# Kernel optimization log

Measured on AMD Instinct MI355X. Metric: run time of the kernel, lower is better.

Reference implementation:

```python
import jax, jax.numpy as jnp
import numpy as np

B, C, H, W, K = 8, 768, 64, 64, 256
EPS = 1e-12  # torch F.normalize eps


def setup_inputs() -> dict:
    key = jax.random.key(0)
    k1, k2 = jax.random.split(key)
    return {
        "x": jax.random.normal(k1, (B, C, H, W), dtype=jnp.float32),
        "centroids": jax.random.normal(k2, (B, C, K), dtype=jnp.float32),
        "sim_alpha": jnp.ones((1,), dtype=jnp.float32),
        "sim_beta": jnp.zeros((1,), dtype=jnp.float32),
    }


def reference(x, centroids, sim_alpha, sim_beta):
    b, c, h, w = x.shape
    n = h * w
    x_r = x.reshape(b, c, n)               # (B,C,N)
    xt = jnp.swapaxes(x_r, 1, 2)           # (B,N,C) tokens
    ct = jnp.swapaxes(centroids, 1, 2)     # (B,K,C) centroids
    # cosine similarity (F.normalize uses max(norm, eps))
    xn = xt / jnp.maximum(jnp.linalg.norm(xt, axis=-1, keepdims=True), EPS)
    cn = ct / jnp.maximum(jnp.linalg.norm(ct, axis=-1, keepdims=True), EPS)
    cos = jnp.einsum('bkc,bnc->bkn', cn, xn)                  # (B,K,N)
    sim = jax.nn.sigmoid(sim_beta + sim_alpha * cos)          # (B,K,N)
    # hard assignment mask: each token kept only for its argmax centroid
    max_idx = jnp.argmax(sim, axis=1)                         # (B,N)
    mask = jnp.swapaxes(jax.nn.one_hot(max_idx, sim.shape[1], dtype=sim.dtype), 1, 2)  # (B,K,N)
    sim_masked = sim * mask                                   # (B,K,N)
    # aggregation: sum over tokens weighted by masked similarity
    agg = jnp.einsum('bkn,bnc->bkc', sim_masked, xt)          # (B,K,C)
    counts = jnp.sum(mask, axis=-1, keepdims=True)            # (B,K,1)
    hyperedges = (agg + ct) / (counts + 1.0)                  # (B,K,C)
    return hyperedges, sim_masked
```

## Files before the change

### kernel.cpp

```cpp
#include <hip/hip_runtime.h>
#include <cmath>

#define Bdim 8
#define Cdim 768
#define Kdim 256
#define Ndim 4096
#define NT 64
#define KC2 32
#define NCH (Cdim / KC2)

typedef __bf16 bf16x8 __attribute__((ext_vector_type(8)));
typedef short  s16x8  __attribute__((ext_vector_type(8)));
typedef float  f32x4  __attribute__((ext_vector_type(4)));
union U8 { s16x8 s; bf16x8 b; };

typedef __attribute__((address_space(1))) const unsigned int g_u32;
typedef __attribute__((address_space(3))) unsigned int l_u32;
__device__ __forceinline__ void gload16(const void* g, void* l) {
    __builtin_amdgcn_global_load_lds((g_u32*)g, (l_u32*)l, 16, 0, 0);
}

__device__ __forceinline__ unsigned short bf16_rne(float f) {
    unsigned u = __float_as_uint(f);
    unsigned r = u + 0x7FFFu + ((u >> 16) & 1u);
    return (unsigned short)(r >> 16);
}
__device__ __forceinline__ float bf2f(unsigned short h) {
    return __uint_as_float((unsigned)h << 16);
}

__device__ __forceinline__ void split3(float v, short& h, short& m, short& l) {
    unsigned u = __float_as_uint(v);
    unsigned th = u + 0x7FFFu + ((u >> 16) & 1u);
    h = (short)(th >> 16);
    float r1 = v - __uint_as_float(th & 0xFFFF0000u);
    unsigned u1 = __float_as_uint(r1);
    unsigned tm = u1 + 0x7FFFu + ((u1 >> 16) & 1u);
    m = (short)(tm >> 16);
    float r2 = r1 - __uint_as_float(tm & 0xFFFF0000u);
    unsigned u2 = __float_as_uint(r2);
    unsigned tl = u2 + 0x7FFFu + ((u2 >> 16) & 1u);
    l = (short)(tl >> 16);
}

__global__ __launch_bounds__(256) void prep_kernel(
    const float* __restrict__ cents, float* __restrict__ invc, int* __restrict__ cnt)
{
    __shared__ float red[4][Kdim];
    const int tid = threadIdx.x;
    const int b = blockIdx.x;
    const float* cb = cents + (size_t)b * Cdim * Kdim;
    const int q = tid & 63, g = tid >> 6;
    float4 ss = make_float4(0.f, 0.f, 0.f, 0.f);
    for (int r = g; r < Cdim; r += 4) {
        float4 v = *(const float4*)(cb + (size_t)r * Kdim + q * 4);
        ss.x = fmaf(v.x, v.x, ss.x); ss.y = fmaf(v.y, v.y, ss.y);
        ss.z = fmaf(v.z, v.z, ss.z); ss.w = fmaf(v.w, v.w, ss.w);
    }
    *(float4*)&red[g][q * 4] = ss;
    __syncthreads();
    float s = red[0][tid] + red[1][tid] + red[2][tid] + red[3][tid];
    invc[b * Kdim + tid] = 1.f / fmaxf(sqrtf(s), 1e-12f);
    cnt[b * Kdim + tid] = 0;
}

__global__ __launch_bounds__(256) void cvt_kernel(
    const float* __restrict__ cents, short* __restrict__ centH,
    short* __restrict__ centM, short* __restrict__ centL)
{
    const int k = threadIdx.x;
    const int bc = blockIdx.x;
    const float* src = cents + ((size_t)(bc / 96) * Cdim + (size_t)(bc % 96) * 8) * Kdim + k;
    s16x8 H, M, L;
    #pragma unroll
    for (int e = 0; e < 8; ++e) {
        short h, m, l;
        split3(src[(size_t)e * Kdim], h, m, l);
        H[e] = h; M[e] = m; L[e] = l;
    }
    ((s16x8*)centH)[(size_t)bc * 256 + k] = H;
    ((s16x8*)centM)[(size_t)bc * 256 + k] = M;
    ((s16x8*)centL)[(size_t)bc * 256 + k] = L;
}

__global__ __launch_bounds__(256) void cvt2_kernel(
    const float* __restrict__ cents, short* __restrict__ centH,
    short* __restrict__ centM, short* __restrict__ centL,
    float* __restrict__ csq)
{
    const int k = threadIdx.x;
    const int bc = blockIdx.x;
    const float* src = cents + ((size_t)(bc / 96) * Cdim + (size_t)(bc % 96) * 8) * Kdim + k;
    s16x8 H, M, L;
    float sq = 0.f;
    #pragma unroll
    for (int e = 0; e < 8; ++e) {
        float v = src[(size_t)e * Kdim];
        sq = fmaf(v, v, sq);
        short h, m, l;
        split3(v, h, m, l);
        H[e] = h; M[e] = m; L[e] = l;
    }
    ((s16x8*)centH)[(size_t)bc * 256 + k] = H;
    ((s16x8*)centM)[(size_t)bc * 256 + k] = M;
    ((s16x8*)centL)[(size_t)bc * 256 + k] = L;
    csq[(size_t)bc * 256 + k] = sq;
}

__global__ __launch_bounds__(256) void nrm_reduce_kernel(
    const float* __restrict__ csq, float* __restrict__ invc, int* __restrict__ cnt)
{
    const int k = threadIdx.x;
    const int b = blockIdx.x;
    const float* p = csq + (size_t)b * 96 * 256 + k;
    float s0 = 0.f, s1 = 0.f, s2 = 0.f, s3 = 0.f;
    #pragma unroll
    for (int j = 0; j < 96; j += 4) {
        s0 += p[(j + 0) * 256];
        s1 += p[(j + 1) * 256];
        s2 += p[(j + 2) * 256];
        s3 += p[(j + 3) * 256];
    }
    float s = ((s0 + s1) + (s2 + s3));
    invc[b * Kdim + k] = 1.f / fmaxf(sqrtf(s), 1e-12f);
    cnt[b * Kdim + k] = 0;
}

__global__ __launch_bounds__(256) void xpose3_kernel(
    const float* __restrict__ x,
    unsigned short* __restrict__ xH, unsigned short* __restrict__ xM,
    unsigned short* __restrict__ xL, float* __restrict__ xn2p)
{
    __shared__ float tile[64][68];
    __shared__ float psum[4][64];
    const int tid = threadIdx.x;
    const int bid = blockIdx.x;
    const int b  = bid / (12 * 64);
    const int r  = bid % (12 * 64);
    const int ct = r / 64, nt = r % 64;
    const float* src = x + ((size_t)b * Cdim + ct * 64) * Ndim + nt * 64;
    #pragma unroll
    for (int it = 0; it < 4; ++it) {
        int idx = tid + it * 256;
        int c = idx >> 4, n4 = idx & 15;
        *(float4*)&tile[c][n4 * 4] = *(const float4*)&src[(size_t)c * Ndim + n4 * 4];
    }
    __syncthreads();

    {
        const int grp = tid >> 6, tn = tid & 63;
        float s = 0.f;
        #pragma unroll
        for (int cc = 0; cc < 16; ++cc) {
            float v = tile[grp * 16 + cc][tn];
            s = fmaf(v, v, s);
        }
        psum[grp][tn] = s;
    }
    __syncthreads();
    if (tid < 64)
        xn2p[((size_t)(b * 12 + ct)) * Ndim + nt * 64 + tid] =
            psum[0][tid] + psum[1][tid] + psum[2][tid] + psum[3][tid];

    #pragma unroll
    for (int it = 0; it < 8; ++it) {
        int idx = tid + it * 256;
        int n = idx >> 5, cp = idx & 31;
        short h0, m0, l0, h1, m1, l1;
        split3(tile[cp * 2][n],     h0, m0, l0);
        split3(tile[cp * 2 + 1][n], h1, m1, l1);
        size_t o = ((size_t)(b * Ndim + nt * 64 + n)) * Cdim + ct * 64 + cp * 2;
        *(unsigned*)&xH[o] = (unsigned)(unsigned short)h0 | ((unsigned)(unsigned short)h1 << 16);
        *(unsigned*)&xM[o] = (unsigned)(unsigned short)m0 | ((unsigned)(unsigned short)m1 << 16);
        *(unsigned*)&xL[o] = (unsigned)(unsigned short)l0 | ((unsigned)(unsigned short)l1 << 16);
    }
}

__global__ __launch_bounds__(256) void xpose_kernel(
    const float* __restrict__ x, unsigned short* __restrict__ xTh)
{
    __shared__ float tile[64][68];
    const int tid = threadIdx.x;
    const int bid = blockIdx.x;
    const int b  = bid / (12 * 64);
    const int r  = bid % (12 * 64);
    const int ct = r / 64, nt = r % 64;
    const float* src = x + ((size_t)b * Cdim + ct * 64) * Ndim + nt * 64;
    #pragma unroll
    for (int it = 0; it < 4; ++it) {
        int idx = tid + it * 256;
        int c = idx >> 4, n4 = idx & 15;
        *(float4*)&tile[c][n4 * 4] = *(const float4*)&src[(size_t)c * Ndim + n4 * 4];
    }
    __syncthreads();
    #pragma unroll
    for (int it = 0; it < 8; ++it) {
        int idx = tid + it * 256;
        int n = idx >> 5, cp = idx & 31;
        unsigned pk = (unsigned)bf16_rne(tile[cp * 2][n])
                    | ((unsigned)bf16_rne(tile[cp * 2 + 1][n]) << 16);
        *(unsigned*)&xTh[((size_t)(b * Ndim + nt * 64 + n)) * Cdim + ct * 64 + cp * 2] = pk;
    }
}

__global__ __launch_bounds__(256) void scan_kernel(
    const int* __restrict__ cnt, const int* __restrict__ kArr,
    int* __restrict__ bucketOff, int* __restrict__ toks)
{
    __shared__ int cS[256];
    __shared__ int offS[256];
    __shared__ int cur[256];
    const int tid = threadIdx.x;
    const int b = blockIdx.x;
    cS[tid] = cnt[b * 256 + tid];
    __syncthreads();
    if (tid == 0) {
        int a = 0;
        for (int k = 0; k < 256; ++k) { offS[k] = a; a += cS[k]; }
    }
    __syncthreads();
    bucketOff[b * 256 + tid] = offS[tid];
    cur[tid] = offS[tid];
    __syncthreads();
    for (int i = tid; i < Ndim; i += 256) {
        int k = kArr[b * Ndim + i];
        int pos = atomicAdd(&cur[k], 1);
        toks[b * Ndim + pos] = i;
    }
}

__global__ __launch_bounds__(192) void aggB_kernel(
    const unsigned short* __restrict__ xTh,
    const float* __restrict__ cents,
    const float* __restrict__ wArr,
    const int* __restrict__ toks,
    const int* __restrict__ bucketOff,
    const int* __restrict__ cnt,
    float* __restrict__ hyp)
{
    const int tid = threadIdx.x;
    const int b  = blockIdx.x >> 7;
    const int kg = blockIdx.x & 127;
    const int t4 = tid * 4;
    #pragma unroll
    for (int j = 0; j < 2; ++j) {
        const int k = kg * 2 + j;
        const int off = bucketOff[b * 256 + k];
        const int num = cnt[b * 256 + k];
        const int base = b * Ndim + off;
        float a0 = 0.f, a1 = 0.f, a2 = 0.f, a3 = 0.f;
        int i = 0;
        for (; i + 4 <= num; i += 4) {
            int na = toks[base + i],     nb = toks[base + i + 1];
            int nc = toks[base + i + 2], nd = toks[base + i + 3];
            float wa = wArr[b * Ndim + na], wb = wArr[b * Ndim + nb];
            float wc = wArr[b * Ndim + nc], wd = wArr[b * Ndim + nd];
            ushort4 ha = *(const ushort4*)&xTh[((size_t)(b * Ndim + na)) * Cdim + t4];
            ushort4 hb = *(const ushort4*)&xTh[((size_t)(b * Ndim + nb)) * Cdim + t4];
            ushort4 hc = *(const ushort4*)&xTh[((size_t)(b * Ndim + nc)) * Cdim + t4];
            ushort4 hd = *(const ushort4*)&xTh[((size_t)(b * Ndim + nd)) * Cdim + t4];
            a0 += wa * bf2f(ha.x) + wb * bf2f(hb.x) + wc * bf2f(hc.x) + wd * bf2f(hd.x);
            a1 += wa * bf2f(ha.y) + wb * bf2f(hb.y) + wc * bf2f(hc.y) + wd * bf2f(hd.y);
            a2 += wa * bf2f(ha.z) + wb * bf2f(hb.z) + wc * bf2f(hc.z) + wd * bf2f(hd.z);
            a3 += wa * bf2f(ha.w) + wb * bf2f(hb.w) + wc * bf2f(hc.w) + wd * bf2f(hd.w);
        }
        for (; i < num; ++i) {
            int n = toks[base + i];
            float w = wArr[b * Ndim + n];
            ushort4 h = *(const ushort4*)&xTh[((size_t)(b * Ndim + n)) * Cdim + t4];
            a0 += w * bf2f(h.x); a1 += w * bf2f(h.y);
            a2 += w * bf2f(h.z); a3 += w * bf2f(h.w);
        }
        float d = (float)(num + 1);
        float4 o;
        o.x = (a0 + cents[((size_t)b * Cdim + t4 + 0) * Kdim + k]) / d;
        o.y = (a1 + cents[((size_t)b * Cdim + t4 + 1) * Kdim + k]) / d;
        o.z = (a2 + cents[((size_t)b * Cdim + t4 + 2) * Kdim + k]) / d;
        o.w = (a3 + cents[((size_t)b * Cdim + t4 + 3) * Kdim + k]) / d;
        *(float4*)&hyp[((size_t)(b * Kdim + k)) * Cdim + t4] = o;
    }
}

#define PASS(Afr, Bfr)                                                        \
    _Pragma("unroll")                                                         \
    for (int kf = 0; kf < 4; ++kf)                                            \
        _Pragma("unroll")                                                     \
        for (int nf = 0; nf < 4; ++nf)                                        \
            acc[kf][nf] = __builtin_amdgcn_mfma_f32_16x16x32_bf16(            \
                Afr[kf].b, Bfr[nf].b, acc[kf][nf], 0, 0, 0);

__global__ __launch_bounds__(256, 2) void sim_stage_kernel(
    const short* __restrict__ xH, const short* __restrict__ xM,
    const short* __restrict__ xL,
    const short* __restrict__ centH, const short* __restrict__ centM,
    const short* __restrict__ centL,
    const float* __restrict__ alpha_p, const float* __restrict__ beta_p,
    const float* __restrict__ invc, const float* __restrict__ xn2p,
    float* __restrict__ simOut, float* __restrict__ wArr,
    int* __restrict__ kArr, int* __restrict__ cnt)
{
    __shared__ __align__(16) s16x8 sB[3][3][256];
    __shared__ float bwv[4][NT];
    __shared__ int   bwk[4][NT];

    const int tid  = threadIdx.x;
    const int lane = tid & 63;
    const int w    = tid >> 6;
    const int q    = lane >> 4;
    const int c15  = lane & 15;
    const int b    = blockIdx.x & 7;
    const int n0   = (blockIdx.x >> 3) * NT;

    const int nloc = w * 16 + (lane >> 2);
    const int rsw  = (lane & 3) ^ ((nloc >> 1) & 3);
    const size_t gsrc = ((size_t)b * Ndim + n0 + nloc) * 96 + rsw;
    const s16x8* xHp = (const s16x8*)xH;
    const s16x8* xMp = (const s16x8*)xM;
    const s16x8* xLp = (const s16x8*)xL;

    #define STAGE(t_) do { const int bf_ = (t_) % 3;                          \
        gload16(xHp + gsrc + (size_t)(t_) * 4, &sB[bf_][0][w * 64]);          \
        gload16(xMp + gsrc + (size_t)(t_) * 4, &sB[bf_][1][w * 64]);          \
        gload16(xLp + gsrc + (size_t)(t_) * 4, &sB[bf_][2][w * 64]);          \
    } while (0)

    const s16x8* cHb = (const s16x8*)centH + (size_t)b * 96 * 256;
    const s16x8* cMb = (const s16x8*)centM + (size_t)b * 96 * 256;
    const s16x8* cLb = (const s16x8*)centL + (size_t)b * 96 * 256;
    const int rowA0 = w * 64 + c15;

    #define LOADA(dstH, dstM, dstL, t_) do {                                  \
        const int ra_ = ((t_) * 4 + q) * 256 + rowA0;                         \
        _Pragma("unroll")                                                     \
        for (int kf = 0; kf < 4; ++kf) {                                      \
            dstH[kf].s = cHb[ra_ + kf * 16];                                  \
            dstM[kf].s = cMb[ra_ + kf * 16];                                  \
            dstL[kf].s = cLb[ra_ + kf * 16];                                  \
        }                                                                     \
    } while (0)

    f32x4 acc[4][4];
    #pragma unroll
    for (int i = 0; i < 4; ++i)
        #pragma unroll
        for (int j = 0; j < 4; ++j) acc[i][j] = (f32x4){0.f, 0.f, 0.f, 0.f};

    U8 aH0[4], aM0[4], aL0[4];
    U8 aH1[4], aM1[4], aL1[4];

    LOADA(aH0, aM0, aL0, 0);
    STAGE(0);
    STAGE(1);

    const int swz = (c15 >> 1) & 3;

    #define CHUNK(t_, aHc, aMc, aLc, aHn, aMn, aLn)                           \
    {                                                                         \
        asm volatile("s_waitcnt vmcnt(3)" ::: "memory");                      \
        __builtin_amdgcn_s_barrier();                                         \
        __builtin_amdgcn_sched_barrier(0);                                    \
        { const int tn_ = ((t_) + 1 < NCH) ? (t_) + 1 : NCH - 1;              \
          LOADA(aHn, aMn, aLn, tn_); }                                        \
        __builtin_amdgcn_sched_barrier(0);                                    \
        if ((t_) + 2 < NCH) STAGE((t_) + 2);                                  \
        const int cur_ = (t_) % 3;                                            \
        U8 bH[4], bM[4], bL[4];                                               \
        _Pragma("unroll")                                                     \
        for (int nf = 0; nf < 4; ++nf) {                                      \
            const int ri = (nf * 16 + c15) * 4 + (q ^ swz);                   \
            bH[nf].s = sB[cur_][0][ri];                                       \
            bM[nf].s = sB[cur_][1][ri];                                       \
            bL[nf].s = sB[cur_][2][ri];                                       \
        }                                                                     \
        PASS(aHc, bH) PASS(aMc, bH) PASS(aLc, bH)                             \
        PASS(aHc, bM) PASS(aMc, bM) PASS(aHc, bL)                             \
    }

    for (int t = 0; t < NCH; t += 2) {
        CHUNK(t,     aH0, aM0, aL0, aH1, aM1, aL1);
        CHUNK(t + 1, aH1, aM1, aL1, aH0, aM0, aL0);
    }
    #undef CHUNK
    #undef LOADA
    #undef STAGE

    const float alpha = alpha_p[0];
    const float beta  = beta_p[0];

    #pragma unroll
    for (int nf = 0; nf < 4; ++nf) {
        const int n = n0 + nf * 16 + c15;
        float xs = 0.f;
        #pragma unroll
        for (int j = 0; j < 12; ++j) xs += xn2p[(size_t)(b * 12 + j) * Ndim + n];
        const float ivx = 1.f / fmaxf(sqrtf(xs), 1e-12f);
        float best = -1.f; int bk = 0;
        #pragma unroll
        for (int kf = 0; kf < 4; ++kf) {
            float4 ic = *(const float4*)&invc[b * Kdim + w * 64 + kf * 16 + q * 4];
            #pragma unroll
            for (int r = 0; r < 4; ++r) {
                float cosv = acc[kf][nf][r] * ((const float*)&ic)[r] * ivx;
                float s = 1.f / (1.f + expf(-(beta + alpha * cosv)));
                int k = w * 64 + kf * 16 + q * 4 + r;
                if (s > best) { best = s; bk = k; }
            }
        }
        #pragma unroll
        for (int off = 16; off < 64; off <<= 1) {
            float ov = __shfl_xor(best, off);
            int   ok = __shfl_xor(bk, off);
            if (ov > best || (ov == best && ok < bk)) { best = ov; bk = ok; }
        }
        if (q == 0) { bwv[w][nf * 16 + c15] = best; bwk[w][nf * 16 + c15] = bk; }
    }
    __syncthreads();
    if (tid < NT) {
        float best = -1.f; int bk = 0;
        #pragma unroll
        for (int g = 0; g < 4; ++g) {
            float v = bwv[g][tid];
            if (v > best) { best = v; bk = bwk[g][tid]; }
        }
        int gn = b * Ndim + n0 + tid;
        wArr[gn] = best;
        kArr[gn] = bk;
        simOut[((size_t)(b * Kdim + bk)) * Ndim + n0 + tid] = best;
        atomicAdd(&cnt[b * Kdim + bk], 1);
    }
}

__global__ __launch_bounds__(256, 2) void sim_mfma_kernel(
    const float* __restrict__ x,
    const short* __restrict__ centH,
    const short* __restrict__ centM,
    const short* __restrict__ centL,
    const float* __restrict__ alpha_p,
    const float* __restrict__ beta_p,
    const float* __restrict__ invc,
    float* __restrict__ simOut,
    float* __restrict__ wArr,
    int*   __restrict__ kArr,
    int*   __restrict__ cnt)
{
    __shared__ __align__(16) float sxf[3][KC2][NT];
    __shared__ float invcS[Kdim];
    __shared__ float px[4][NT];
    __shared__ float invxS[NT];
    __shared__ float bwv[4][NT];
    __shared__ int   bwk[4][NT];

    const int tid  = threadIdx.x;
    const int lane = tid & 63;
    const int w    = tid >> 6;
    const int q    = lane >> 4;
    const int c15  = lane & 15;
    const int b    = blockIdx.x >> 6;
    const int n0   = (blockIdx.x & 63) * NT;
    const float* xb = x + (size_t)b * Cdim * Ndim;

    invcS[tid] = invc[b * Kdim + tid];
    const float alpha = alpha_p[0];
    const float beta  = beta_p[0];

    f32x4 acc[4][4];
    #pragma unroll
    for (int i = 0; i < 4; ++i)
        #pragma unroll
        for (int j = 0; j < 4; ++j) acc[i][j] = (f32x4){0.f, 0.f, 0.f, 0.f};

    float xn2p_ = 0.f;

    #define STAGE(t_) do {                                                    \
        const int bf_ = (t_) % 3; const int c0_ = (t_) * KC2;                 \
        _Pragma("unroll")                                                     \
        for (int i_ = 0; i_ < 2; ++i_)                                        \
            gload16(xb + (size_t)(c0_ + w * 8 + i_ * 4 + q) * Ndim            \
                       + n0 + c15 * 4,                                        \
                    &sxf[bf_][w * 8 + i_ * 4][0]);                            \
    } while (0)

    STAGE(0);
    STAGE(1);

    const s16x8* cHb = (const s16x8*)centH + ((size_t)b * 96) * 256;
    const s16x8* cMb = (const s16x8*)centM + ((size_t)b * 96) * 256;
    const s16x8* cLb = (const s16x8*)centL + ((size_t)b * 96) * 256;

    for (int t = 0; t < NCH; ++t) {
        asm volatile("s_waitcnt vmcnt(2)" ::: "memory");
        __builtin_amdgcn_s_barrier();
        __builtin_amdgcn_sched_barrier(0);

        const int cur = t % 3;

        U8 aH[4], aM[4], aL[4];
        {
            const size_t rowb = ((size_t)(t * 4 + q)) * 256 + w * 64 + c15;
            #pragma unroll
            for (int kf = 0; kf < 4; ++kf) {
                aH[kf].s = cHb[rowb + kf * 16];
                aM[kf].s = cMb[rowb + kf * 16];
                aL[kf].s = cLb[rowb + kf * 16];
            }
        }
        if (t + 2 < NCH) STAGE(t + 2);

        #pragma unroll
        for (int r = 0; r < 8; ++r) {
            float v = sxf[cur][w * 8 + r][lane];
            xn2p_ = fmaf(v, v, xn2p_);
        }

        U8 bH[4], bM[4], bL[4];
        #pragma unroll
        for (int nf = 0; nf < 4; ++nf) {
            #pragma unroll
            for (int e = 0; e < 8; ++e) {
                short h, m, l;
                split3(sxf[cur][q * 8 + e][nf * 16 + c15], h, m, l);
                bH[nf].s[e] = h; bM[nf].s[e] = m; bL[nf].s[e] = l;
            }
        }

        PASS(aH, bH) PASS(aH, bM) PASS(aM, bH)
        PASS(aH, bL) PASS(aL, bH) PASS(aM, bM)
    }
    #undef STAGE

    __syncthreads();
    px[w][lane] = xn2p_;
    __syncthreads();
    if (tid < NT) {
        float s = px[0][tid] + px[1][tid] + px[2][tid] + px[3][tid];
        invxS[tid] = 1.f / fmaxf(sqrtf(s), 1e-12f);
    }
    __syncthreads();

    #pragma unroll
    for (int nf = 0; nf < 4; ++nf) {
        const float ivx = invxS[nf * 16 + c15];
        float best = -1.f; int bk = 0;
        #pragma unroll
        for (int kf = 0; kf < 4; ++kf) {
            float4 ic = *(const float4*)&invcS[w * 64 + kf * 16 + q * 4];
            #pragma unroll
            for (int r = 0; r < 4; ++r) {
                float cosv = acc[kf][nf][r] * ((const float*)&ic)[r] * ivx;
                float s = 1.f / (1.f + expf(-(beta + alpha * cosv)));
                int k = w * 64 + kf * 16 + q * 4 + r;
                if (s > best) { best = s; bk = k; }
            }
        }
        #pragma unroll
        for (int off = 16; off < 64; off <<= 1) {
            float ov = __shfl_xor(best, off);
            int   ok = __shfl_xor(bk, off);
            if (ov > best || (ov == best && ok < bk)) { best = ov; bk = ok; }
        }
        if (q == 0) { bwv[w][nf * 16 + c15] = best; bwk[w][nf * 16 + c15] = bk; }
    }
    __syncthreads();
    if (tid < NT) {
        float best = -1.f; int bk = 0;
        #pragma unroll
        for (int g = 0; g < 4; ++g) {
            float v = bwv[g][tid];
            if (v > best) { best = v; bk = bwk[g][tid]; }
        }
        int gn = b * Ndim + n0 + tid;
        wArr[gn] = best;
        kArr[gn] = bk;
        simOut[((size_t)(b * Kdim + bk)) * Ndim + n0 + tid] = best;
        atomicAdd(&cnt[b * Kdim + bk], 1);
    }
}

extern "C" void kernel_launch(void* const* d_in, const int* in_sizes, int n_in,
                              void* d_out, int out_size, void* d_ws, size_t ws_size,
                              hipStream_t stream)
{
    const float* x     = (const float*)d_in[0];
    const float* cents = (const float*)d_in[1];
    const float* alpha = (const float*)d_in[2];
    const float* beta  = (const float*)d_in[3];

    float* hyp    = (float*)d_out;
    float* simOut = (float*)d_out + (size_t)Bdim * Kdim * Cdim;

    char* ws = (char*)d_ws;
    hipMemsetAsync(simOut, 0, (size_t)Bdim * Kdim * Ndim * sizeof(float), stream);

    const size_t WS_FULL = 163209216ull;
    const size_t WS_R13  = 60186624ull;

    if (ws_size >= WS_FULL) {
        float* wArr  = (float*)(ws);
        int*   kArr  = (int*)  (ws + 131072);
        int*   cnt   = (int*)  (ws + 262144);
        float* invc  = (float*)(ws + 270336);
        float* xn2p  = (float*)(ws + 278528);
        short* centH = (short*)(ws + 1851392);
        short* centM = (short*)(ws + 4997120);
        short* centL = (short*)(ws + 8142848);
        int*   toks  = (int*)  (ws + 11288576);
        int*   boff  = (int*)  (ws + 11419648);
        unsigned short* xH = (unsigned short*)(ws + 11427840);
        unsigned short* xM = (unsigned short*)(ws + 61759488);
        unsigned short* xL = (unsigned short*)(ws + 112091136);
        float* csq   = (float*)(ws + 162422784);

        cvt2_kernel<<<dim3(Bdim * 96), dim3(256), 0, stream>>>(
            cents, centH, centM, centL, csq);
        nrm_reduce_kernel<<<dim3(Bdim), dim3(256), 0, stream>>>(csq, invc, cnt);
        xpose3_kernel<<<dim3(Bdim * 12 * 64), dim3(256), 0, stream>>>(x, xH, xM, xL, xn2p);
        sim_stage_kernel<<<dim3(Bdim * (Ndim / NT)), dim3(256), 0, stream>>>(
            (const short*)xH, (const short*)xM, (const short*)xL,
            centH, centM, centL, alpha, beta, invc, xn2p,
            simOut, wArr, kArr, cnt);
        scan_kernel<<<dim3(Bdim), dim3(256), 0, stream>>>(cnt, kArr, boff, toks);
        aggB_kernel<<<dim3(Bdim * 128), dim3(192), 0, stream>>>(
            xH, cents, wArr, toks, boff, cnt, hyp);
    } else if (ws_size >= WS_R13) {
        float* wArr  = (float*)(ws);
        int*   kArr  = (int*)  (ws + 131072);
        int*   cnt   = (int*)  (ws + 262144);
        float* invc  = (float*)(ws + 270336);
        short* centH = (short*)(ws + 278528);
        short* centM = (short*)(ws + 3424256);
        short* centL = (short*)(ws + 6569984);
        int*   toks  = (int*)  (ws + 9715712);
        int*   boff  = (int*)  (ws + 9846784);
        unsigned short* xTh = (unsigned short*)(ws + 9854976);

        prep_kernel<<<dim3(Bdim), dim3(256), 0, stream>>>(cents, invc, cnt);
        cvt_kernel<<<dim3(Bdim * 96), dim3(256), 0, stream>>>(cents, centH, centM, centL);
        xpose_kernel<<<dim3(Bdim * 12 * 64), dim3(256), 0, stream>>>(x, xTh);
        sim_mfma_kernel<<<dim3(Bdim * (Ndim / NT)), dim3(256), 0, stream>>>(
            x, centH, centM, centL, alpha, beta, invc, simOut, wArr, kArr, cnt);
        scan_kernel<<<dim3(Bdim), dim3(256), 0, stream>>>(cnt, kArr, boff, toks);
        aggB_kernel<<<dim3(Bdim * 128), dim3(192), 0, stream>>>(
            xTh, cents, wArr, toks, boff, cnt, hyp);
    }
}
```

Baseline: 170.4 us.

## Halve sim tile to 32 tokens and write full masked sim rows in-kernel

The similarity kernel now processes 32 tokens per block instead of 64. This doubles the grid, raises the occupancy hint to 3, and gives each wave one x plane to stage. The kernel also writes the whole dense sim_masked column itself, zeros included, so the separate 32 MB memset of the sim output is dropped on this path. This trades a memset pass for strided in-kernel stores and reloads the centroid fragments twice as often per token.

```diff
diff --git a/kernel.cpp b/kernel.cpp
--- a/kernel.cpp
+++ b/kernel.cpp
@@ -6,6 +6,7 @@
 #define Kdim 256
 #define Ndim 4096
 #define NT 64
+#define NT2 32
 #define KC2 32
 #define NCH (Cdim / KC2)
 
@@ -281,6 +282,14 @@
     }
 }
 
+#define PASS2(Afr, Bfr)                                                       \
+    _Pragma("unroll")                                                         \
+    for (int kf = 0; kf < 4; ++kf)                                            \
+        _Pragma("unroll")                                                     \
+        for (int nf = 0; nf < 2; ++nf)                                        \
+            acc[kf][nf] = __builtin_amdgcn_mfma_f32_16x16x32_bf16(            \
+                Afr[kf].b, Bfr[nf].b, acc[kf][nf], 0, 0, 0);
+
 #define PASS(Afr, Bfr)                                                        \
     _Pragma("unroll")                                                         \
     for (int kf = 0; kf < 4; ++kf)                                            \
@@ -289,7 +298,7 @@
             acc[kf][nf] = __builtin_amdgcn_mfma_f32_16x16x32_bf16(            \
                 Afr[kf].b, Bfr[nf].b, acc[kf][nf], 0, 0, 0);
 
-__global__ __launch_bounds__(256, 2) void sim_stage_kernel(
+__global__ __launch_bounds__(256, 3) void sim_stage32_kernel(
     const short* __restrict__ xH, const short* __restrict__ xM,
     const short* __restrict__ xL,
     const short* __restrict__ centH, const short* __restrict__ centM,
@@ -299,9 +308,11 @@
     float* __restrict__ simOut, float* __restrict__ wArr,
     int* __restrict__ kArr, int* __restrict__ cnt)
 {
-    __shared__ __align__(16) s16x8 sB[3][3][256];
-    __shared__ float bwv[4][NT];
-    __shared__ int   bwk[4][NT];
+    __shared__ __align__(16) s16x8 sB[3][3][128];
+    __shared__ float bwv[4][NT2];
+    __shared__ int   bwk[4][NT2];
+    __shared__ float wbestS[NT2];
+    __shared__ int   kstarS[NT2];
 
     const int tid  = threadIdx.x;
     const int lane = tid & 63;
@@ -309,19 +320,19 @@
     const int q    = lane >> 4;
     const int c15  = lane & 15;
     const int b    = blockIdx.x & 7;
-    const int n0   = (blockIdx.x >> 3) * NT;
-
-    const int nloc = w * 16 + (lane >> 2);
-    const int rsw  = (lane & 3) ^ ((nloc >> 1) & 3);
-    const size_t gsrc = ((size_t)b * Ndim + n0 + nloc) * 96 + rsw;
-    const s16x8* xHp = (const s16x8*)xH;
-    const s16x8* xMp = (const s16x8*)xM;
-    const s16x8* xLp = (const s16x8*)xL;
+    const int n0   = (blockIdx.x >> 3) * NT2;
+
+    const int we = (w == 3) ? 0 : w;
+    const s16x8* myplane = (we == 0) ? (const s16x8*)xH
+                         : (we == 1) ? (const s16x8*)xM : (const s16x8*)xL;
+    const int nl0 = (lane >> 2);
+    const int nl1 = 16 + (lane >> 2);
+    const size_t gs0 = ((size_t)b * Ndim + n0 + nl0) * 96 + ((lane & 3) ^ ((nl0 >> 1) & 3));
+    const size_t gs1 = ((size_t)b * Ndim + n0 + nl1) * 96 + ((lane & 3) ^ ((nl1 >> 1) & 3));
 
     #define STAGE(t_) do { const int bf_ = (t_) % 3;                          \
-        gload16(xHp + gsrc + (size_t)(t_) * 4, &sB[bf_][0][w * 64]);          \
-        gload16(xMp + gsrc + (size_t)(t_) * 4, &sB[bf_][1][w * 64]);          \
-        gload16(xLp + gsrc + (size_t)(t_) * 4, &sB[bf_][2][w * 64]);          \
+        gload16(myplane + gs0 + (size_t)(t_) * 4, &sB[bf_][we][0]);           \
+        gload16(myplane + gs1 + (size_t)(t_) * 4, &sB[bf_][we][64]);          \
     } while (0)
 
     const s16x8* cHb = (const s16x8*)centH + (size_t)b * 96 * 256;
@@ -339,11 +350,11 @@
         }                                                                     \
     } while (0)
 
-    f32x4 acc[4][4];
+    f32x4 acc[4][2];
     #pragma unroll
     for (int i = 0; i < 4; ++i)
         #pragma unroll
-        for (int j = 0; j < 4; ++j) acc[i][j] = (f32x4){0.f, 0.f, 0.f, 0.f};
+        for (int j = 0; j < 2; ++j) acc[i][j] = (f32x4){0.f, 0.f, 0.f, 0.f};
 
     U8 aH0[4], aM0[4], aL0[4];
     U8 aH1[4], aM1[4], aL1[4];
@@ -356,7 +367,7 @@
 
     #define CHUNK(t_, aHc, aMc, aLc, aHn, aMn, aLn)                           \
     {                                                                         \
-        asm volatile("s_waitcnt vmcnt(3)" ::: "memory");                      \
+        asm volatile("s_waitcnt vmcnt(2)" ::: "memory");                      \
         __builtin_amdgcn_s_barrier();                                         \
         __builtin_amdgcn_sched_barrier(0);                                    \
         { const int tn_ = ((t_) + 1 < NCH) ? (t_) + 1 : NCH - 1;              \
@@ -364,16 +375,16 @@
         __builtin_amdgcn_sched_barrier(0);                                    \
         if ((t_) + 2 < NCH) STAGE((t_) + 2);                                  \
         const int cur_ = (t_) % 3;                                            \
-        U8 bH[4], bM[4], bL[4];                                               \
+        U8 bH[2], bM[2], bL[2];                                               \
         _Pragma("unroll")                                                     \
-        for (int nf = 0; nf < 4; ++nf) {                                      \
+        for (int nf = 0; nf < 2; ++nf) {                                      \
             const int ri = (nf * 16 + c15) * 4 + (q ^ swz);                   \
             bH[nf].s = sB[cur_][0][ri];                                       \
             bM[nf].s = sB[cur_][1][ri];                                       \
             bL[nf].s = sB[cur_][2][ri];                                       \
         }                                                                     \
-        PASS(aHc, bH) PASS(aMc, bH) PASS(aLc, bH)                             \
-        PASS(aHc, bM) PASS(aMc, bM) PASS(aHc, bL)                             \
+        PASS2(aHc, bH) PASS2(aMc, bH) PASS2(aLc, bH)                          \
+        PASS2(aHc, bM) PASS2(aMc, bM) PASS2(aHc, bL)                          \
     }
 
     for (int t = 0; t < NCH; t += 2) {
@@ -388,7 +399,7 @@
     const float beta  = beta_p[0];
 
     #pragma unroll
-    for (int nf = 0; nf < 4; ++nf) {
+    for (int nf = 0; nf < 2; ++nf) {
         const int n = n0 + nf * 16 + c15;
         float xs = 0.f;
         #pragma unroll
@@ -415,7 +426,7 @@
         if (q == 0) { bwv[w][nf * 16 + c15] = best; bwk[w][nf * 16 + c15] = bk; }
     }
     __syncthreads();
-    if (tid < NT) {
+    if (tid < NT2) {
         float best = -1.f; int bk = 0;
         #pragma unroll
         for (int g = 0; g < 4; ++g) {
@@ -425,8 +436,22 @@
         int gn = b * Ndim + n0 + tid;
         wArr[gn] = best;
         kArr[gn] = bk;
-        simOut[((size_t)(b * Kdim + bk)) * Ndim + n0 + tid] = best;
+        wbestS[tid] = best;
+        kstarS[tid] = bk;
         atomicAdd(&cnt[b * Kdim + bk], 1);
+    }
+    __syncthreads();
+
+    {
+        const int nn = lane & 31;
+        const int kst = kstarS[nn];
+        const float wbs = wbestS[nn];
+        float* base = simOut + ((size_t)(b * Kdim + w * 64 + (lane >> 5))) * Ndim + n0 + nn;
+        #pragma unroll
+        for (int it = 0; it < 32; ++it) {
+            int row = w * 64 + it * 2 + (lane >> 5);
+            base[(size_t)(it * 2) * Ndim] = (row == kst) ? wbs : 0.f;
+        }
     }
 }
 
@@ -589,7 +614,6 @@
     float* simOut = (float*)d_out + (size_t)Bdim * Kdim * Cdim;
 
     char* ws = (char*)d_ws;
-    hipMemsetAsync(simOut, 0, (size_t)Bdim * Kdim * Ndim * sizeof(float), stream);
 
     const size_t WS_FULL = 163209216ull;
     const size_t WS_R13  = 60186624ull;
@@ -614,7 +638,7 @@
             cents, centH, centM, centL, csq);
         nrm_reduce_kernel<<<dim3(Bdim), dim3(256), 0, stream>>>(csq, invc, cnt);
         xpose3_kernel<<<dim3(Bdim * 12 * 64), dim3(256), 0, stream>>>(x, xH, xM, xL, xn2p);
-        sim_stage_kernel<<<dim3(Bdim * (Ndim / NT)), dim3(256), 0, stream>>>(
+        sim_stage32_kernel<<<dim3(Bdim * (Ndim / NT2)), dim3(256), 0, stream>>>(
             (const short*)xH, (const short*)xM, (const short*)xL,
             centH, centM, centL, alpha, beta, invc, xn2p,
             simOut, wArr, kArr, cnt);
@@ -633,6 +657,7 @@
         int*   boff  = (int*)  (ws + 9846784);
         unsigned short* xTh = (unsigned short*)(ws + 9854976);
 
+        hipMemsetAsync(simOut, 0, (size_t)Bdim * Kdim * Ndim * sizeof(float), stream);
         prep_kernel<<<dim3(Bdim), dim3(256), 0, stream>>>(cents, invc, cnt);
         cvt_kernel<<<dim3(Bdim * 96), dim3(256), 0, stream>>>(cents, centH, centM, centL);
         xpose_kernel<<<dim3(Bdim * 12 * 64), dim3(256), 0, stream>>>(x, xTh);
```

Measured after the change: 177.8 us. 1.04x slower.

## Load token fragments directly into registers instead of staging through LDS

Applied to the files above, without the earlier changes.

The similarity GEMM kernel no longer stages the x (token) tiles through a triple-buffered LDS ring with global_load_lds and per-chunk barriers. Each wave now loads its own B fragments from global memory into registers, double-buffered one chunk ahead. The centroid A fragments are loaded per chunk without prefetch. MFMA passes are also wrapped in s_setprio. This removes LDS traffic and the block barrier, but every wave now re-reads the same token data from global/L2 and the A loads are exposed, which adds memory traffic and latency.

```diff
diff --git a/kernel.cpp b/kernel.cpp
--- a/kernel.cpp
+++ b/kernel.cpp
@@ -289,7 +289,7 @@
             acc[kf][nf] = __builtin_amdgcn_mfma_f32_16x16x32_bf16(            \
                 Afr[kf].b, Bfr[nf].b, acc[kf][nf], 0, 0, 0);
 
-__global__ __launch_bounds__(256, 2) void sim_stage_kernel(
+__global__ __launch_bounds__(256, 2) void sim_reg_kernel(
     const short* __restrict__ xH, const short* __restrict__ xM,
     const short* __restrict__ xL,
     const short* __restrict__ centH, const short* __restrict__ centM,
@@ -299,7 +299,6 @@
     float* __restrict__ simOut, float* __restrict__ wArr,
     int* __restrict__ kArr, int* __restrict__ cnt)
 {
-    __shared__ __align__(16) s16x8 sB[3][3][256];
     __shared__ float bwv[4][NT];
     __shared__ int   bwk[4][NT];
 
@@ -311,78 +310,67 @@
     const int b    = blockIdx.x & 7;
     const int n0   = (blockIdx.x >> 3) * NT;
 
-    const int nloc = w * 16 + (lane >> 2);
-    const int rsw  = (lane & 3) ^ ((nloc >> 1) & 3);
-    const size_t gsrc = ((size_t)b * Ndim + n0 + nloc) * 96 + rsw;
     const s16x8* xHp = (const s16x8*)xH;
     const s16x8* xMp = (const s16x8*)xM;
     const s16x8* xLp = (const s16x8*)xL;
-
-    #define STAGE(t_) do { const int bf_ = (t_) % 3;                          \
-        gload16(xHp + gsrc + (size_t)(t_) * 4, &sB[bf_][0][w * 64]);          \
-        gload16(xMp + gsrc + (size_t)(t_) * 4, &sB[bf_][1][w * 64]);          \
-        gload16(xLp + gsrc + (size_t)(t_) * 4, &sB[bf_][2][w * 64]);          \
-    } while (0)
+    size_t rB[4];
+    #pragma unroll
+    for (int nf = 0; nf < 4; ++nf)
+        rB[nf] = ((size_t)b * Ndim + n0 + nf * 16 + c15) * 96 + q;
 
     const s16x8* cHb = (const s16x8*)centH + (size_t)b * 96 * 256;
     const s16x8* cMb = (const s16x8*)centM + (size_t)b * 96 * 256;
     const s16x8* cLb = (const s16x8*)centL + (size_t)b * 96 * 256;
     const int rowA0 = w * 64 + c15;
 
-    #define LOADA(dstH, dstM, dstL, t_) do {                                  \
-        const int ra_ = ((t_) * 4 + q) * 256 + rowA0;                         \
+    #define LOADB(BH, BM, BL, t_) do {                                        \
         _Pragma("unroll")                                                     \
-        for (int kf = 0; kf < 4; ++kf) {                                      \
-            dstH[kf].s = cHb[ra_ + kf * 16];                                  \
-            dstM[kf].s = cMb[ra_ + kf * 16];                                  \
-            dstL[kf].s = cLb[ra_ + kf * 16];                                  \
+        for (int nf = 0; nf < 4; ++nf) BH[nf].s = xHp[rB[nf] + (t_) * 4];     \
+        _Pragma("unroll")                                                     \
+        for (int nf = 0; nf < 4; ++nf) BM[nf].s = xMp[rB[nf] + (t_) * 4];     \
+        _Pragma("unroll")                                                     \
+        for (int nf = 0; nf < 4; ++nf) BL[nf].s = xLp[rB[nf] + (t_) * 4];     \
+    } while (0)
+
+    f32x4 acc[4][4];
+    #pragma unroll
+    for (int i = 0; i < 4; ++i)
+        #pragma unroll
+        for (int j = 0; j < 4; ++j) acc[i][j] = (f32x4){0.f, 0.f, 0.f, 0.f};
+
+    U8 bH0[4], bM0[4], bL0[4];
+    U8 bH1[4], bM1[4], bL1[4];
+
+    LOADB(bH0, bM0, bL0, 0);
+
+    #define CHUNK(t_, BHc, BMc, BLc, BHn, BMn, BLn)                           \
+    {                                                                         \
+        __builtin_amdgcn_sched_barrier(0);                                    \
+        U8 aH[4], aM[4], aL[4];                                               \
+        {   const int ra_ = ((t_) * 4 + q) * 256 + rowA0;                     \
+            _Pragma("unroll")                                                 \
+            for (int kf = 0; kf < 4; ++kf) {                                  \
+                aH[kf].s = cHb[ra_ + kf * 16];                                \
+                aM[kf].s = cMb[ra_ + kf * 16];                                \
+                aL[kf].s = cLb[ra_ + kf * 16];                                \
+            }                                                                 \
         }                                                                     \
-    } while (0)
-
-    f32x4 acc[4][4];
-    #pragma unroll
-    for (int i = 0; i < 4; ++i)
-        #pragma unroll
-        for (int j = 0; j < 4; ++j) acc[i][j] = (f32x4){0.f, 0.f, 0.f, 0.f};
-
-    U8 aH0[4], aM0[4], aL0[4];
-    U8 aH1[4], aM1[4], aL1[4];
-
-    LOADA(aH0, aM0, aL0, 0);
-    STAGE(0);
-    STAGE(1);
-
-    const int swz = (c15 >> 1) & 3;
-
-    #define CHUNK(t_, aHc, aMc, aLc, aHn, aMn, aLn)                           \
-    {                                                                         \
-        asm volatile("s_waitcnt vmcnt(3)" ::: "memory");                      \
-        __builtin_amdgcn_s_barrier();                                         \
         __builtin_amdgcn_sched_barrier(0);                                    \
         { const int tn_ = ((t_) + 1 < NCH) ? (t_) + 1 : NCH - 1;              \
-          LOADA(aHn, aMn, aLn, tn_); }                                        \
+          LOADB(BHn, BMn, BLn, tn_); }                                        \
         __builtin_amdgcn_sched_barrier(0);                                    \
-        if ((t_) + 2 < NCH) STAGE((t_) + 2);                                  \
-        const int cur_ = (t_) % 3;                                            \
-        U8 bH[4], bM[4], bL[4];                                               \
-        _Pragma("unroll")                                                     \
-        for (int nf = 0; nf < 4; ++nf) {                                      \
-            const int ri = (nf * 16 + c15) * 4 + (q ^ swz);                   \
-            bH[nf].s = sB[cur_][0][ri];                                       \
-            bM[nf].s = sB[cur_][1][ri];                                       \
-            bL[nf].s = sB[cur_][2][ri];                                       \
-        }                                                                     \
-        PASS(aHc, bH) PASS(aMc, bH) PASS(aLc, bH)                             \
-        PASS(aHc, bM) PASS(aMc, bM) PASS(aHc, bL)                             \
+        __builtin_amdgcn_s_setprio(1);                                        \
+        PASS(aH, BHc) PASS(aM, BHc) PASS(aL, BHc)                             \
+        PASS(aH, BMc) PASS(aM, BMc) PASS(aH, BLc)                             \
+        __builtin_amdgcn_s_setprio(0);                                        \
     }
 
     for (int t = 0; t < NCH; t += 2) {
-        CHUNK(t,     aH0, aM0, aL0, aH1, aM1, aL1);
-        CHUNK(t + 1, aH1, aM1, aL1, aH0, aM0, aL0);
+        CHUNK(t,     bH0, bM0, bL0, bH1, bM1, bL1);
+        CHUNK(t + 1, bH1, bM1, bL1, bH0, bM0, bL0);
     }
     #undef CHUNK
-    #undef LOADA
-    #undef STAGE
+    #undef LOADB
 
     const float alpha = alpha_p[0];
     const float beta  = beta_p[0];
@@ -614,7 +602,7 @@
             cents, centH, centM, centL, csq);
         nrm_reduce_kernel<<<dim3(Bdim), dim3(256), 0, stream>>>(csq, invc, cnt);
         xpose3_kernel<<<dim3(Bdim * 12 * 64), dim3(256), 0, stream>>>(x, xH, xM, xL, xn2p);
-        sim_stage_kernel<<<dim3(Bdim * (Ndim / NT)), dim3(256), 0, stream>>>(
+        sim_reg_kernel<<<dim3(Bdim * (Ndim / NT)), dim3(256), 0, stream>>>(
             (const short*)xH, (const short*)xM, (const short*)xL,
             centH, centM, centL, alpha, beta, invc, xn2p,
             simOut, wArr, kArr, cnt);
```

Result: slower. 194.5 us (+14.1%).
